# Kernel tuning notes

Hardware: AMD Instinct MI355X
Metric: run time of the kernel (lower is better)

## Reference

```python
import jax, jax.numpy as jnp
import numpy as np

B, C, L, H = 2, 512, 4096, 8
D = C // H  # depth per head


def setup_inputs() -> dict:
    key = jax.random.key(0)
    k1, k2, k3 = jax.random.split(key, 3)
    queries = jax.random.normal(k1, (B, C, L), dtype=jnp.float32)
    mask = jnp.ones((B, L), dtype=jnp.int32)
    # xavier-ish scaling for stability
    Wm = jax.random.normal(k2, (2 * C, C), dtype=jnp.float32) * (1.0 / np.sqrt(C))
    Wq = jax.random.normal(k3, (C, C), dtype=jnp.float32) * (1.0 / np.sqrt(C))
    return {"queries": queries, "mask": mask, "Wm": Wm, "Wq": Wq}


def reference(queries, mask, Wm, Wq):
    # 1x1 conv projections == channel matmuls on [B, C, L]
    q = jnp.einsum('oc,bcl->bol', Wq, queries)   # [B, C, L]
    m = jnp.einsum('oc,bcl->bol', Wm, queries)   # [B, 2C, L]
    # to [B, L, *], split heads -> [B, H, L, D]
    qh = q.transpose(0, 2, 1).reshape(B, L, H, D).transpose(0, 2, 1, 3)
    mem = m.transpose(0, 2, 1)                   # [B, L, 2C]
    k, v = jnp.split(mem, 2, axis=2)             # each [B, L, C]
    kh = k.reshape(B, L, H, D).transpose(0, 2, 1, 3)
    vh = v.reshape(B, L, H, D).transpose(0, 2, 1, 3)
    qh = qh * (D ** -0.5)
    logits = jnp.einsum('bhqd,bhkd->bhqk', qh, kh)          # [B, H, L, L]
    mf = mask.astype(jnp.float32)[:, None, None, :]          # [B, 1, 1, L]
    logits = logits + (-1e30) * (1.0 - mf)
    weights = jax.nn.softmax(logits, axis=-1)                # dropout is identity in eval
    out = jnp.einsum('bhqk,bhkd->bhqd', weights, vh)         # [B, H, L, D]
    # combine heads -> [B, L, C] -> [B, C, L]
    return out.transpose(0, 2, 1, 3).reshape(B, L, C).transpose(0, 2, 1)
```

## Files before the change

### kernel.cpp

```cpp
#include <hip/hip_runtime.h>

#define Bn 2
#define Cn 512
#define Ln 4096
#define Hn 8
#define Dn 64

typedef _Float16 f16;
typedef _Float16 h8 __attribute__((ext_vector_type(8)));
typedef _Float16 h4 __attribute__((ext_vector_type(4)));
typedef float f32x4 __attribute__((ext_vector_type(4)));
typedef float f32x16 __attribute__((ext_vector_type(16)));

#define MFMA32(a, b, c) __builtin_amdgcn_mfma_f32_16x16x32_f16(a, b, c, 0, 0, 0)
#define MFMA3216(a, b, c) __builtin_amdgcn_mfma_f32_32x32x16_f16(a, b, c, 0, 0, 0)
#define AS1(p) ((const __attribute__((address_space(1))) void*)(p))
#define AS3(p) ((__attribute__((address_space(3))) void*)(p))

__global__ __launch_bounds__(256) void k_transpose(const float* __restrict__ X,
                                                   f16* __restrict__ Xt) {
  int bid = blockIdx.x;
  int b  = bid >> 9;
  int r  = bid & 511;
  int lt = r >> 3, ct = r & 7;
  int l0 = lt << 6, c0 = ct << 6;
  __shared__ f16 t[64][66];
  int tid = threadIdx.x;
  int lx = tid & 63, cg = tid >> 6;
  const float* xb = X + ((size_t)b * Cn) * Ln;
#pragma unroll
  for (int rr = 0; rr < 16; ++rr) {
    int cl = cg * 16 + rr;
    t[lx][cl] = (f16)xb[(size_t)(c0 + cl) * Ln + l0 + lx];
  }
  __syncthreads();
  f16* xo = Xt + ((size_t)b * Ln + l0) * Cn + c0;
  int cx = tid & 63, lg = tid >> 6;
#pragma unroll
  for (int rr = 0; rr < 16; ++rr) {
    int ll = lg * 16 + rr;
    xo[(size_t)ll * Cn + cx] = t[ll][cx];
  }
}

__global__ __launch_bounds__(256) void k_proj(const float* __restrict__ Wq,
                                              const float* __restrict__ Wm,
                                              const f16* __restrict__ Xt,
                                              f16* __restrict__ Qd,
                                              f16* __restrict__ Kd,
                                              f16* __restrict__ Vv) {
  int bid = blockIdx.x;
  int b = bid / 384;
  int r = bid % 384;
  int mt = r >> 5, nt = r & 31;
  int o0 = mt << 7, l0 = nt << 7;
  __shared__ f16 a_lds[128][40];
  __shared__ f16 b_lds[128][40];
  int tid = threadIdx.x;
  int lane = tid & 63, w = tid >> 6;
  int wr = w >> 1, wc = w & 1;
  f32x4 acc[4][4] = {};

  int sr = tid >> 1;
  int scg = (tid & 1) << 4;
  int o_s = o0 + sr;
  const float* wrow = (o_s < 512) ? (Wq + (size_t)o_s * Cn)
                                  : (Wm + (size_t)(o_s - 512) * Cn);
  const f16* xrow = Xt + ((size_t)b * Ln + l0 + sr) * Cn;

  for (int kt = 0; kt < 16; ++kt) {
    int c0 = kt << 5;
    __syncthreads();
#pragma unroll
    for (int i = 0; i < 4; ++i) {
      float4 w4 = *(const float4*)(wrow + c0 + scg + 4 * i);
      h4 hh = { (f16)w4.x, (f16)w4.y, (f16)w4.z, (f16)w4.w };
      *(h4*)&a_lds[sr][scg + 4 * i] = hh;
    }
#pragma unroll
    for (int i = 0; i < 2; ++i)
      *(h8*)&b_lds[sr][scg + 8 * i] = *(const h8*)(xrow + c0 + scg + 8 * i);
    __syncthreads();

    h8 af[4], bf[4];
#pragma unroll
    for (int mi = 0; mi < 4; ++mi)
      af[mi] = *(const h8*)&a_lds[wr * 64 + mi * 16 + (lane & 15)][(lane >> 4) * 8];
#pragma unroll
    for (int ni = 0; ni < 4; ++ni)
      bf[ni] = *(const h8*)&b_lds[wc * 64 + ni * 16 + (lane & 15)][(lane >> 4) * 8];
#pragma unroll
    for (int mi = 0; mi < 4; ++mi)
#pragma unroll
      for (int ni = 0; ni < 4; ++ni)
        acc[mi][ni] = MFMA32(af[mi], bf[ni], acc[mi][ni]);
  }

  const float QSCALE = 0.18033688011112042f;
  int lrow = (lane >> 4) << 2;
  int lcol = lane & 15;
#pragma unroll
  for (int mi = 0; mi < 4; ++mi) {
    int ob = o0 + wr * 64 + mi * 16 + lrow;
#pragma unroll
    for (int ni = 0; ni < 4; ++ni) {
      int lc = l0 + wc * 64 + ni * 16 + lcol;
      f32x4 a = acc[mi][ni];
      if (ob < 512) {
        int h = ob >> 6, d = ob & 63;
        h4 hh = { (f16)(a[0] * QSCALE), (f16)(a[1] * QSCALE),
                  (f16)(a[2] * QSCALE), (f16)(a[3] * QSCALE) };
        *(h4*)&Qd[(((size_t)b * Hn + h) * Ln + lc) * Dn + d] = hh;
      } else if (ob < 1024) {
        int oc = ob - 512;
        int h = oc >> 6, d = oc & 63;
        h4 hh = { (f16)a[0], (f16)a[1], (f16)a[2], (f16)a[3] };
        *(h4*)&Kd[(((size_t)b * Hn + h) * Ln + lc) * Dn + d] = hh;
      } else {
        int oc = ob - 1024;
#pragma unroll
        for (int rr = 0; rr < 4; ++rr)
          Vv[((size_t)b * Cn + oc + rr) * Ln + lc] = (f16)a[rr];
      }
    }
  }
}

__global__ __launch_bounds__(512, 4) void k_attn(const f16* __restrict__ Qd,
                                                 const f16* __restrict__ Kd,
                                                 const f16* __restrict__ Vv,
                                                 const int* __restrict__ mask,
                                                 float* __restrict__ out) {
  int bid0 = blockIdx.x;
  int bid = (bid0 & 7) * 64 + (bid0 >> 3);
  int bh = bid >> 5, ib = bid & 31;
  int b = bh >> 3, h = bh & 7;
  int tid = threadIdx.x;
  int lane = tid & 63, w = tid >> 6;
  int grp = w >> 2, wq = w & 3;
  int il = lane & 31, hi = lane >> 5;

  __shared__ __align__(16) f16 smem[8 * 4096];
#define KBUF(g, bi) (&smem[(((g) * 2 + (bi))) * 4096])
#define VBUF(g, bi) (&smem[((4 + (g) * 2 + (bi))) * 4096])

  int qb = ib * 128 + wq * 32;
  const f16* qp = Qd + ((size_t)bh * Ln + qb + il) * Dn;
  h8 qreg[4];
#pragma unroll
  for (int dt = 0; dt < 4; ++dt)
    qreg[dt] = *(const h8*)(qp + dt * 16 + hi * 8);

  const int* mbase = mask + (size_t)b * Ln;
  unsigned long long flags;
  {
    const int4* mp = (const int4*)mbase + lane * 16;
    int ac = 1;
#pragma unroll
    for (int q = 0; q < 16; ++q) { int4 v = mp[q]; ac &= v.x & v.y & v.z & v.w; }
    flags = __ballot(ac == 1);
  }

  const f16* kbase = Kd + (size_t)bh * Ln * Dn + (size_t)grp * 32 * 4096;
  const f16* vbase = Vv + ((size_t)b * Cn + h * 64) * Ln + grp * 32 * 64;
  int koff[2], voff[2];
#pragma unroll
  for (int q = 0; q < 2; ++q) {
    int rr = wq * 16 + q * 8 + (lane >> 3);
    int swz = (lane & 7) ^ (rr & 7);
    koff[q] = rr * 64 + swz * 8;
    voff[q] = rr * Ln + swz * 8;
  }

#define STAGE(bi, t)                                                            \
  {                                                                             \
    _Pragma("unroll")                                                           \
    for (int q = 0; q < 2; ++q) {                                               \
      __builtin_amdgcn_global_load_lds(AS1(kbase + (size_t)(t) * 4096 + koff[q]),\
                                       AS3(KBUF(grp, bi) + (wq * 16 + q * 8) * 64),\
                                       16, 0, 0);                               \
      __builtin_amdgcn_global_load_lds(AS1(vbase + (size_t)(t) * 64 + voff[q]), \
                                       AS3(VBUF(grp, bi) + (wq * 16 + q * 8) * 64),\
                                       16, 0, 0);                               \
    }                                                                           \
  }

  f32x16 acc0 = {}, acc1 = {};
  float mrow = -1e38f;
  float lsum = 0.f;
  int swz7 = il & 7;

  STAGE(0, 0);
  STAGE(1, 1);

#define BODY(t_, waitn_)                                                        \
  {                                                                             \
    asm volatile("s_waitcnt vmcnt(" waitn_ ")" ::: "memory");                   \
    __builtin_amdgcn_s_barrier();                                               \
    const f16* kl_ = KBUF(grp, (t_) & 1);                                       \
    f32x16 s0 = {}, s1 = {};                                                    \
    __builtin_amdgcn_s_setprio(1);                                              \
    _Pragma("unroll")                                                           \
    for (int dt = 0; dt < 4; ++dt) {                                            \
      int c = ((dt * 2 + hi) ^ swz7) << 3;                                      \
      h8 ak0 = *(const h8*)&kl_[il * 64 + c];                                   \
      h8 ak1 = *(const h8*)&kl_[(32 + il) * 64 + c];                            \
      s0 = MFMA3216(ak0, qreg[dt], s0);                                         \
      s1 = MFMA3216(ak1, qreg[dt], s1);                                         \
    }                                                                           \
    __builtin_amdgcn_s_setprio(0);                                              \
    int T_ = grp * 32 + (t_);                                                   \
    if (!((flags >> T_) & 1)) {                                                 \
      _Pragma("unroll")                                                         \
      for (int r = 0; r < 16; ++r) {                                            \
        int j = T_ * 64 + (r & 3) + 8 * (r >> 2) + 4 * hi;                      \
        if (!mbase[j])      s0[r] = -3.0e4f;                                    \
        if (!mbase[j + 32]) s1[r] = -3.0e4f;                                    \
      }                                                                         \
    }                                                                           \
    float m0 = fmaxf(fmaxf(s0[0], s0[1]), fmaxf(s0[2], s0[3]));                 \
    float m1 = fmaxf(fmaxf(s0[4], s0[5]), fmaxf(s0[6], s0[7]));                 \
    float m2 = fmaxf(fmaxf(s0[8], s0[9]), fmaxf(s0[10], s0[11]));               \
    float m3 = fmaxf(fmaxf(s0[12], s0[13]), fmaxf(s0[14], s0[15]));             \
    float m4 = fmaxf(fmaxf(s1[0], s1[1]), fmaxf(s1[2], s1[3]));                 \
    float m5 = fmaxf(fmaxf(s1[4], s1[5]), fmaxf(s1[6], s1[7]));                 \
    float m6 = fmaxf(fmaxf(s1[8], s1[9]), fmaxf(s1[10], s1[11]));               \
    float m7 = fmaxf(fmaxf(s1[12], s1[13]), fmaxf(s1[14], s1[15]));             \
    float mx = fmaxf(fmaxf(fmaxf(m0, m1), fmaxf(m2, m3)),                       \
                     fmaxf(fmaxf(m4, m5), fmaxf(m6, m7)));                      \
    mx = fmaxf(mx, __shfl_xor(mx, 32));                                         \
    if (__any(mx > mrow + 8.f)) {                     \
      float mn = fmaxf(mrow, mx);                                               \
      float al = __builtin_amdgcn_exp2f(mrow - mn);                             \
      lsum *= al;                                                               \
      _Pragma("unroll")                                                         \
      for (int r = 0; r < 16; ++r) { acc0[r] *= al; acc1[r] *= al; }            \
      mrow = mn;                                                                \
    }                                                                           \
    _Pragma("unroll")                                                           \
    for (int r = 0; r < 16; ++r) {                                              \
      s0[r] = __builtin_amdgcn_exp2f(s0[r] - mrow);                             \
      s1[r] = __builtin_amdgcn_exp2f(s1[r] - mrow);                             \
    }                                                                           \
    {                                                    \
      float a0 = (s0[0] + s0[1]) + (s0[2] + s0[3]);                             \
      float a1 = (s0[4] + s0[5]) + (s0[6] + s0[7]);                             \
      float a2 = (s0[8] + s0[9]) + (s0[10] + s0[11]);                           \
      float a3 = (s0[12] + s0[13]) + (s0[14] + s0[15]);                         \
      float a4 = (s1[0] + s1[1]) + (s1[2] + s1[3]);                             \
      float a5 = (s1[4] + s1[5]) + (s1[6] + s1[7]);                             \
      float a6 = (s1[8] + s1[9]) + (s1[10] + s1[11]);                           \
      float a7 = (s1[12] + s1[13]) + (s1[14] + s1[15]);                         \
      float rs = ((a0 + a1) + (a2 + a3)) + ((a4 + a5) + (a6 + a7));             \
      rs += __shfl_xor(rs, 32);                                                 \
      lsum += rs;                                                               \
    }                                                                           \
    float dw0[8], dw1[8];                                                       \
    _Pragma("unroll")                                                           \
    for (int r = 0; r < 16; r += 2) {                                           \
      dw0[r >> 1] = __builtin_bit_cast(float,                                   \
          __builtin_amdgcn_cvt_pkrtz(s0[r], s0[r + 1]));                        \
      dw1[r >> 1] = __builtin_bit_cast(float,                                   \
          __builtin_amdgcn_cvt_pkrtz(s1[r], s1[r + 1]));                        \
    }                                                                           \
    h8 pb[4];                                                                   \
    _Pragma("unroll")                                                           \
    for (int jt = 0; jt < 4; ++jt) {                                            \
      const float* dd = (jt < 2) ? dw0 : dw1;                                   \
      int base = (jt & 1) * 4;                                                  \
      float x0 = dd[base + 0], x1 = dd[base + 1];                               \
      float y0 = dd[base + 2], y1 = dd[base + 3];                               \
      float v0 = hi ? x0 : y0, v1 = hi ? x1 : y1;                               \
      float p0 = __shfl_xor(v0, 32), p1 = __shfl_xor(v1, 32);                   \
      union { h8 v; float f[4]; } u;                                            \
      u.f[0] = hi ? p0 : x0;                                                    \
      u.f[1] = hi ? p1 : x1;                                                    \
      u.f[2] = hi ? y0 : p0;                                                    \
      u.f[3] = hi ? y1 : p1;                                                    \
      pb[jt] = u.v;                                                             \
    }                                                                           \
    const f16* vl_ = VBUF(grp, (t_) & 1);                                       \
    __builtin_amdgcn_s_setprio(1);                                              \
    _Pragma("unroll")                                                           \
    for (int dt = 0; dt < 2; ++dt) {                                            \
      int rv = dt * 32 + il;                                                    \
      _Pragma("unroll")                                                         \
      for (int jt = 0; jt < 4; ++jt) {                                          \
        h8 av = *(const h8*)&vl_[rv * 64 + (((jt * 2 + hi) ^ swz7) << 3)];      \
        if (dt == 0) acc0 = MFMA3216(av, pb[jt], acc0);                         \
        else         acc1 = MFMA3216(av, pb[jt], acc1);                         \
      }                                                                         \
    }                                                                           \
    __builtin_amdgcn_s_setprio(0);                                              \
    __builtin_amdgcn_s_barrier();                                               \
    if ((t_) < 30) STAGE((t_) & 1, (t_) + 2);                                   \
  }

  for (int t = 0; t < 31; ++t) {
    BODY(t, "4");
  }
  BODY(31, "0");

  __syncthreads();
  float* shf = (float*)smem;
  if (grp == 1) {
    float* basep = shf + wq * (64 * 33) + lane * 33;
#pragma unroll
    for (int r = 0; r < 16; ++r) { basep[r] = acc0[r]; basep[16 + r] = acc1[r]; }
    float* ml = shf + 4 * 64 * 33 + (wq * 64 + lane) * 2;
    ml[0] = mrow; ml[1] = lsum;
  }
  __syncthreads();
  if (grp == 0) {
    float* basep = shf + wq * (64 * 33) + lane * 33;
    float* ml = shf + 4 * 64 * 33 + (wq * 64 + lane) * 2;
    float mB = ml[0], lB = ml[1];
    float M = fmaxf(mrow, mB);
    float wA = __builtin_amdgcn_exp2f(mrow - M);
    float wB = __builtin_amdgcn_exp2f(mB - M);
    float linv = 1.f / (lsum * wA + lB * wB);
    float fA = wA * linv, fB = wB * linv;
    size_t obase = ((size_t)b * Cn + h * 64) * Ln + qb + il;
#pragma unroll
    for (int r = 0; r < 16; ++r) {
      int d0 = (r & 3) + 8 * (r >> 2) + 4 * hi;
      out[obase + (size_t)d0 * Ln] = acc0[r] * fA + basep[r] * fB;
      out[obase + (size_t)(d0 + 32) * Ln] = acc1[r] * fA + basep[16 + r] * fB;
    }
  }
}

extern "C" void kernel_launch(void* const* d_in, const int* in_sizes, int n_in,
                              void* d_out, int out_size, void* d_ws, size_t ws_size,
                              hipStream_t stream) {
  const float* queries = (const float*)d_in[0];
  const int*   mask    = (const int*)d_in[1];
  const float* Wm      = (const float*)d_in[2];
  const float* Wq      = (const float*)d_in[3];
  float* out = (float*)d_out;
  char* ws = (char*)d_ws;
  f16* Xt = (f16*)(ws);
  f16* Qd = (f16*)(ws + 8388608);
  f16* Kd = (f16*)(ws + 16777216);
  f16* Vv = (f16*)(ws + 25165824);

  k_transpose<<<1024, 256, 0, stream>>>(queries, Xt);
  k_proj<<<768, 256, 0, stream>>>(Wq, Wm, Xt, Qd, Kd, Vv);
  k_attn<<<512, 512, 0, stream>>>(Qd, Kd, Vv, mask, out);
}
```

Before: 140.6 us.

## Replace per-tile row max with lazy power-of-two rescale triggered by row sum

Removes the per-tile max reduction and cross-lane shuffle from the online softmax. The running offset starts at zero, and the row sum of the exponentials is checked after exp. Only when it exceeds a threshold are P, the accumulators and lsum rescaled by an exact power of two taken from the max's exponent. The P packing now uses v_permlane32_swap instead of shfl plus selects, and the row-sum cross-half reduction moves out of the loop to the end. This risks fp16 overflow or underflow in P if logits grow large, and adds a guard against a zero denominator.

Result: faster. 137.3 us (-2.3%).

```diff
diff --git a/kernel.cpp b/kernel.cpp
--- a/kernel.cpp
+++ b/kernel.cpp
@@ -185,8 +185,31 @@
     }                                                                           \
   }
 
+#define PACK_PB(S0_, S1_, DW0_, DW1_, PB_)                                      \
+  {                                                                             \
+    _Pragma("unroll")                                                           \
+    for (int r = 0; r < 16; r += 2) {                                           \
+      DW0_[r >> 1] = __builtin_bit_cast(float,                                  \
+          __builtin_amdgcn_cvt_pkrtz(S0_[r], S0_[r + 1]));                      \
+      DW1_[r >> 1] = __builtin_bit_cast(float,                                  \
+          __builtin_amdgcn_cvt_pkrtz(S1_[r], S1_[r + 1]));                      \
+    }                                                                           \
+    _Pragma("unroll")                                                           \
+    for (int jt = 0; jt < 4; ++jt) {                                            \
+      float* dd = (jt < 2) ? DW0_ : DW1_;                                       \
+      int base = (jt & 1) * 4;                                                  \
+      float a0 = dd[base + 0], b0 = dd[base + 2];                               \
+      float a1 = dd[base + 1], b1 = dd[base + 3];                               \
+      asm("v_permlane32_swap_b32 %0, %1" : "+v"(a0), "+v"(b0));                 \
+      asm("v_permlane32_swap_b32 %0, %1" : "+v"(a1), "+v"(b1));                 \
+      union { h8 v; float f[4]; } u;                                            \
+      u.f[0] = a0; u.f[1] = a1; u.f[2] = b0; u.f[3] = b1;                       \
+      PB_[jt] = u.v;                                                            \
+    }                                                                           \
+  }
+
   f32x16 acc0 = {}, acc1 = {};
-  float mrow = -1e38f;
+  float mrow = 0.f;
   float lsum = 0.f;
   int swz7 = il & 7;
 
@@ -218,31 +241,16 @@
         if (!mbase[j + 32]) s1[r] = -3.0e4f;                                    \
       }                                                                         \
     }                                                                           \
-    float m0 = fmaxf(fmaxf(s0[0], s0[1]), fmaxf(s0[2], s0[3]));                 \
-    float m1 = fmaxf(fmaxf(s0[4], s0[5]), fmaxf(s0[6], s0[7]));                 \
-    float m2 = fmaxf(fmaxf(s0[8], s0[9]), fmaxf(s0[10], s0[11]));               \
-    float m3 = fmaxf(fmaxf(s0[12], s0[13]), fmaxf(s0[14], s0[15]));             \
-    float m4 = fmaxf(fmaxf(s1[0], s1[1]), fmaxf(s1[2], s1[3]));                 \
-    float m5 = fmaxf(fmaxf(s1[4], s1[5]), fmaxf(s1[6], s1[7]));                 \
-    float m6 = fmaxf(fmaxf(s1[8], s1[9]), fmaxf(s1[10], s1[11]));               \
-    float m7 = fmaxf(fmaxf(s1[12], s1[13]), fmaxf(s1[14], s1[15]));             \
-    float mx = fmaxf(fmaxf(fmaxf(m0, m1), fmaxf(m2, m3)),                       \
-                     fmaxf(fmaxf(m4, m5), fmaxf(m6, m7)));                      \
-    mx = fmaxf(mx, __shfl_xor(mx, 32));                                         \
-    if (__any(mx > mrow + 8.f)) {                     \
-      float mn = fmaxf(mrow, mx);                                               \
-      float al = __builtin_amdgcn_exp2f(mrow - mn);                             \
-      lsum *= al;                                                               \
-      _Pragma("unroll")                                                         \
-      for (int r = 0; r < 16; ++r) { acc0[r] *= al; acc1[r] *= al; }            \
-      mrow = mn;                                                                \
-    }                                                                           \
     _Pragma("unroll")                                                           \
     for (int r = 0; r < 16; ++r) {                                              \
       s0[r] = __builtin_amdgcn_exp2f(s0[r] - mrow);                             \
       s1[r] = __builtin_amdgcn_exp2f(s1[r] - mrow);                             \
     }                                                                           \
-    {                                                    \
+    float dw0[8], dw1[8];                                                       \
+    h8 pb[4];                                                                   \
+    PACK_PB(s0, s1, dw0, dw1, pb);                                              \
+    float rs;                                                                   \
+    {                   \
       float a0 = (s0[0] + s0[1]) + (s0[2] + s0[3]);                             \
       float a1 = (s0[4] + s0[5]) + (s0[6] + s0[7]);                             \
       float a2 = (s0[8] + s0[9]) + (s0[10] + s0[11]);                           \
@@ -251,34 +259,33 @@
       float a5 = (s1[4] + s1[5]) + (s1[6] + s1[7]);                             \
       float a6 = (s1[8] + s1[9]) + (s1[10] + s1[11]);                           \
       float a7 = (s1[12] + s1[13]) + (s1[14] + s1[15]);                         \
-      float rs = ((a0 + a1) + (a2 + a3)) + ((a4 + a5) + (a6 + a7));             \
-      rs += __shfl_xor(rs, 32);                                                 \
-      lsum += rs;                                                               \
-    }                                                                           \
-    float dw0[8], dw1[8];                                                       \
-    _Pragma("unroll")                                                           \
-    for (int r = 0; r < 16; r += 2) {                                           \
-      dw0[r >> 1] = __builtin_bit_cast(float,                                   \
-          __builtin_amdgcn_cvt_pkrtz(s0[r], s0[r + 1]));                        \
-      dw1[r >> 1] = __builtin_bit_cast(float,                                   \
-          __builtin_amdgcn_cvt_pkrtz(s1[r], s1[r + 1]));                        \
-    }                                                                           \
-    h8 pb[4];                                                                   \
-    _Pragma("unroll")                                                           \
-    for (int jt = 0; jt < 4; ++jt) {                                            \
-      const float* dd = (jt < 2) ? dw0 : dw1;                                   \
-      int base = (jt & 1) * 4;                                                  \
-      float x0 = dd[base + 0], x1 = dd[base + 1];                               \
-      float y0 = dd[base + 2], y1 = dd[base + 3];                               \
-      float v0 = hi ? x0 : y0, v1 = hi ? x1 : y1;                               \
-      float p0 = __shfl_xor(v0, 32), p1 = __shfl_xor(v1, 32);                   \
-      union { h8 v; float f[4]; } u;                                            \
-      u.f[0] = hi ? p0 : x0;                                                    \
-      u.f[1] = hi ? p1 : x1;                                                    \
-      u.f[2] = hi ? y0 : p0;                                                    \
-      u.f[3] = hi ? y1 : p1;                                                    \
-      pb[jt] = u.v;                                                             \
-    }                                                                           \
+      rs = ((a0 + a1) + (a2 + a3)) + ((a4 + a5) + (a6 + a7));                   \
+    }                                                                           \
+    if (__any(rs > 8192.f)) {   \
+      float mxp = fmaxf(                                                        \
+        fmaxf(fmaxf(fmaxf(s0[0], s0[1]), fmaxf(s0[2], s0[3])),                  \
+              fmaxf(fmaxf(s0[4], s0[5]), fmaxf(s0[6], s0[7]))),                 \
+        fmaxf(fmaxf(fmaxf(s0[8], s0[9]), fmaxf(s0[10], s0[11])),                \
+              fmaxf(fmaxf(s0[12], s0[13]), fmaxf(s0[14], s0[15]))));            \
+      float mxq = fmaxf(                                                        \
+        fmaxf(fmaxf(fmaxf(s1[0], s1[1]), fmaxf(s1[2], s1[3])),                  \
+              fmaxf(fmaxf(s1[4], s1[5]), fmaxf(s1[6], s1[7]))),                 \
+        fmaxf(fmaxf(fmaxf(s1[8], s1[9]), fmaxf(s1[10], s1[11])),                \
+              fmaxf(fmaxf(s1[12], s1[13]), fmaxf(s1[14], s1[15]))));            \
+      mxp = fmaxf(mxp, mxq);                                                    \
+      mxp = fmaxf(mxp, __shfl_xor(mxp, 32));                   \
+      int e = (((__builtin_bit_cast(int, mxp) >> 23) & 255) - 127) - 3;         \
+      float sc = __builtin_bit_cast(float, (127 - e) << 23);    \
+      mrow += (float)e;                                                         \
+      _Pragma("unroll")                                                         \
+      for (int r = 0; r < 16; ++r) {                                            \
+        s0[r] *= sc; s1[r] *= sc;                                               \
+        acc0[r] *= sc; acc1[r] *= sc;                                           \
+      }                                                                         \
+      lsum *= sc; rs *= sc;                                                     \
+      PACK_PB(s0, s1, dw0, dw1, pb);                                            \
+    }                                                                           \
+    lsum += rs;                                                                 \
     const f16* vl_ = VBUF(grp, (t_) & 1);                                       \
     __builtin_amdgcn_s_setprio(1);                                              \
     _Pragma("unroll")                                                           \
@@ -301,6 +308,8 @@
   }
   BODY(31, "0");
 
+  lsum += __shfl_xor(lsum, 32);
+
   __syncthreads();
   float* shf = (float*)smem;
   if (grp == 1) {
@@ -318,7 +327,7 @@
     float M = fmaxf(mrow, mB);
     float wA = __builtin_amdgcn_exp2f(mrow - M);
     float wB = __builtin_amdgcn_exp2f(mB - M);
-    float linv = 1.f / (lsum * wA + lB * wB);
+    float linv = 1.f / fmaxf(lsum * wA + lB * wB, 1e-30f);
     float fA = wA * linv, fB = wB * linv;
     size_t obase = ((size_t)b * Cn + h * 64) * Ln + qb + il;
 #pragma unroll
```
